# Optimization experiments

Measured on AMD Instinct MI355X. Metric: run time of the kernel, lower is better.

Reference implementation:

```python
import jax, jax.numpy as jnp
import numpy as np

B, S, D, H = 4, 1024, 1024, 16
DH = D // H  # head_dim = 64


def setup_inputs() -> dict:
    key = jax.random.key(0)
    kq, kk, kv, kl, kwq, kwk, kwv, kwo = jax.random.split(key, 8)
    query = jax.random.normal(kq, (B, S, D), dtype=jnp.float32)
    key_t = jax.random.normal(kk, (B, S, D), dtype=jnp.float32)
    value = jax.random.normal(kv, (B, S, D), dtype=jnp.float32)
    # padding: keys at positions >= valid length are padded (True)
    lengths = jax.random.randint(kl, (B,), S // 2, S + 1)
    key_padding_mask = jnp.arange(S)[None, :] >= lengths[:, None]  # [B,S] bool
    scale = 1.0 / np.sqrt(D)
    Wq = jax.random.normal(kwq, (D, D), dtype=jnp.float32) * scale
    Wk = jax.random.normal(kwk, (D, D), dtype=jnp.float32) * scale
    Wv = jax.random.normal(kwv, (D, D), dtype=jnp.float32) * scale
    Wo = jax.random.normal(kwo, (D, D), dtype=jnp.float32) * scale
    gamma = jnp.ones((H,), dtype=jnp.float32)
    return {"query": query, "key": key_t, "value": value,
            "key_padding_mask": key_padding_mask,
            "Wq": Wq, "Wk": Wk, "Wv": Wv, "Wo": Wo, "gamma": gamma}


def reference(query, key, value, key_padding_mask, Wq, Wk, Wv, Wo, gamma):
    # nn.Linear(x) = x @ W.T (bias=False)
    q = jnp.einsum('bsd,ed->bse', query, Wq).reshape(B, S, H, DH).transpose(0, 2, 1, 3)  # [B,H,S,Dh]
    k = jnp.einsum('bsd,ed->bse', key, Wk).reshape(B, S, H, DH).transpose(0, 2, 1, 3)
    v = jnp.einsum('bsd,ed->bse', value, Wv).reshape(B, S, H, DH).transpose(0, 2, 1, 3)
    scores = jnp.einsum('bhqd,bhkd->bhqk', q, k) / jnp.sqrt(jnp.float32(DH))
    pad = key_padding_mask[:, None, None, :]  # [B,1,1,S]
    scores = jnp.where(pad, -jnp.inf, scores)
    v = jnp.where(key_padding_mask[:, None, :, None], 0.0, v)
    attn = jax.nn.softmax(scores, axis=-1)  # dropout p=0 (eval) -> identity
    ws = jnp.einsum('bhqk,bhkd->bhqd', attn, v)
    ws = ws * gamma[None, :, None, None]  # per-head scale
    ws = ws.transpose(0, 2, 1, 3).reshape(B, S, D)
    return jnp.einsum('bsd,ed->bse', ws, Wo)
```

## Files before the change

### kernel.cpp

```cpp
#include <hip/hip_runtime.h>
#include <math.h>

#define S_LEN 1024
#define DMODEL 1024

typedef __attribute__((ext_vector_type(8))) short bf16x8;
typedef __attribute__((ext_vector_type(4))) short bf16x4;
typedef __attribute__((ext_vector_type(4))) float f32x4;

#define MFMA16(a, b, c) __builtin_amdgcn_mfma_f32_16x16x32_bf16(a, b, c, 0, 0, 0)

#define WP (1024u * 1024u)
#define XP (4u * 1024u * 1024u)

__device__ __forceinline__ unsigned short rne_bf16(float f) {
    unsigned u = __float_as_uint(f);
    u += 0x7FFFu + ((u >> 16) & 1u);
    return (unsigned short)(u >> 16);
}

__device__ __forceinline__ void split_rne(float f, unsigned short& h, unsigned short& l) {
    unsigned short hh = rne_bf16(f);
    float lf = f - __uint_as_float(((unsigned)hh) << 16);
    h = hh;
    l = rne_bf16(lf);
}

typedef const __attribute__((address_space(1))) unsigned int* gas_t;
typedef __attribute__((address_space(3))) unsigned int* las_t;
__device__ __forceinline__ void glds16(const void* g, void* l) {
    __builtin_amdgcn_global_load_lds((gas_t)g, (las_t)l, 16, 0, 0);
}

__global__ __launch_bounds__(256)
void convert_wx(const float* __restrict__ W0, const float* __restrict__ W1,
                const float* __restrict__ W2, const float* __restrict__ W3,
                const float* __restrict__ Xq, const float* __restrict__ Xk,
                const float* __restrict__ Xv,
                unsigned short* __restrict__ Wpl, unsigned short* __restrict__ Xbase) {
    int blk = blockIdx.x;
    if (blk < 4096) {
        const int which = blk >> 10;
        const float* W = which == 0 ? W0 : which == 1 ? W1 : which == 2 ? W2 : W3;
        int i = ((blk & 1023) * 256 + threadIdx.x) * 4;
        float4 f = *(const float4*)&W[i];
        if (which == 3) {
            unsigned short* hi = Wpl + 3 * WP;
            unsigned short* lo = Wpl + 4 * WP;
            bf16x4 h, l;
            unsigned short hh, ll;
            split_rne(f.x, hh, ll); h[0] = (short)hh; l[0] = (short)ll;
            split_rne(f.y, hh, ll); h[1] = (short)hh; l[1] = (short)ll;
            split_rne(f.z, hh, ll); h[2] = (short)hh; l[2] = (short)ll;
            split_rne(f.w, hh, ll); h[3] = (short)hh; l[3] = (short)ll;
            *(bf16x4*)&hi[i] = h;
            *(bf16x4*)&lo[i] = l;
        } else {
            unsigned short* hi = Wpl + (size_t)which * WP;
            bf16x4 h;
            h[0] = (short)rne_bf16(f.x);
            h[1] = (short)rne_bf16(f.y);
            h[2] = (short)rne_bf16(f.z);
            h[3] = (short)rne_bf16(f.w);
            *(bf16x4*)&hi[i] = h;
        }
    } else {
        blk -= 4096;
        const int which = blk >> 12;
        const float* X = which == 0 ? Xq : which == 1 ? Xk : Xv;
        unsigned short* Xr = Xbase + (size_t)which * XP;
        int i = ((blk & 4095) * 256 + threadIdx.x) * 4;
        float4 f = *(const float4*)&X[i];
        bf16x4 h;
        h[0] = (short)rne_bf16(f.x);
        h[1] = (short)rne_bf16(f.y);
        h[2] = (short)rne_bf16(f.z);
        h[3] = (short)rne_bf16(f.w);
        *(bf16x4*)&Xr[i] = h;
    }
}

__global__ __launch_bounds__(256)
void gemm_proj(const unsigned short* __restrict__ Xbase,
               const unsigned short* __restrict__ Wpl,
               unsigned short* __restrict__ Obase) {
    __shared__ unsigned short AS[128 * 32];
    __shared__ unsigned short BS[128 * 32];

    const int z = blockIdx.z;
    const unsigned short* A = Xbase + (size_t)z * XP;
    const unsigned short* B = Wpl + (size_t)z * WP;

    const int t = threadIdx.x, lane = t & 63, w = t >> 6;
    const int quad = lane >> 4, l15 = lane & 15;
    const int wr = w & 1, wc = w >> 1;
    const int rowBase = blockIdx.y * 128, colBase = blockIdx.x * 128;

    const unsigned short* gA[2];
    const unsigned short* gB[2];
    unsigned short* lA[2];
    unsigned short* lB[2];
    #pragma unroll
    for (int e = 0; e < 2; e++) {
        int row = w * 32 + e * 16 + (lane >> 2);
        int cg = (lane & 3) ^ ((row >> 1) & 3);
        gA[e] = A + (size_t)(rowBase + row) * 1024 + cg * 8;
        gB[e] = B + (size_t)(colBase + row) * 1024 + cg * 8;
        lA[e] = &AS[(w * 32 + e * 16) * 32];
        lB[e] = &BS[(w * 32 + e * 16) * 32];
    }

    int aAd[4], bAd[4];
    #pragma unroll
    for (int i = 0; i < 4; i++) {
        int ra = wr * 64 + i * 16 + l15;
        aAd[i] = ra * 32 + (quad ^ ((ra >> 1) & 3)) * 8;
        int rb = wc * 64 + i * 16 + l15;
        bAd[i] = rb * 32 + (quad ^ ((rb >> 1) & 3)) * 8;
    }

    f32x4 acc[4][4] = {};

    for (int kt = 0; kt < 32; kt++) {
        if (kt) __syncthreads();
        const int ko = kt * 32;
        glds16(gA[0] + ko, lA[0]);
        glds16(gA[1] + ko, lA[1]);
        glds16(gB[0] + ko, lB[0]);
        glds16(gB[1] + ko, lB[1]);
        __syncthreads();

        bf16x8 af[4], bfr[4];
        #pragma unroll
        for (int i = 0; i < 4; i++) af[i] = *(const bf16x8*)&AS[aAd[i]];
        #pragma unroll
        for (int j = 0; j < 4; j++) bfr[j] = *(const bf16x8*)&BS[bAd[j]];
        #pragma unroll
        for (int j = 0; j < 4; j++)
            #pragma unroll
            for (int i = 0; i < 4; i++)
                acc[i][j] = MFMA16(af[i], bfr[j], acc[i][j]);
    }

    unsigned short* O = Obase + (size_t)z * XP;
    #pragma unroll
    for (int i = 0; i < 4; i++)
        #pragma unroll
        for (int j = 0; j < 4; j++)
            #pragma unroll
            for (int r = 0; r < 4; r++) {
                int m = rowBase + wr * 64 + i * 16 + quad * 4 + r;
                int n = colBase + wc * 64 + j * 16 + l15;
                int bb = m >> 10, s = m & 1023, hh = n >> 6, dh = n & 63;
                size_t hb = ((size_t)(bb * 16 + hh)) << 16;
                unsigned short v = rne_bf16(acc[i][j][r]);
                if (z == 2) O[hb + (size_t)dh * 1024 + s] = v;
                else        O[hb + s * 64 + dh] = v;
            }
}

__global__ __launch_bounds__(256)
void gemm_out2(const unsigned short* __restrict__ A,
               const unsigned short* __restrict__ Bh, const unsigned short* __restrict__ Bl,
               float* __restrict__ Cf) {
    __shared__ unsigned short AS[128 * 32];
    __shared__ unsigned short BhS[64 * 32], BlS[64 * 32];

    const int t = threadIdx.x, lane = t & 63, w = t >> 6;
    const int quad = lane >> 4, l15 = lane & 15;
    const int wr = w & 1, wc = w >> 1;
    const int rowBase = blockIdx.y * 128, colBase = blockIdx.x * 64;

    const unsigned short* gA[2];
    unsigned short* lA[2];
    #pragma unroll
    for (int e = 0; e < 2; e++) {
        int row = w * 32 + e * 16 + (lane >> 2);
        int cg = (lane & 3) ^ ((row >> 1) & 3);
        gA[e] = A + (size_t)(rowBase + row) * 1024 + cg * 8;
        lA[e] = &AS[(w * 32 + e * 16) * 32];
    }
    const unsigned short *gBh, *gBl;
    unsigned short *lBh, *lBl;
    {
        int row = w * 16 + (lane >> 2);
        int cg = (lane & 3) ^ ((row >> 1) & 3);
        gBh = Bh + (size_t)(colBase + row) * 1024 + cg * 8;
        gBl = Bl + (size_t)(colBase + row) * 1024 + cg * 8;
        lBh = &BhS[(w * 16) * 32];
        lBl = &BlS[(w * 16) * 32];
    }

    int aAd[4], bAd[2];
    #pragma unroll
    for (int i = 0; i < 4; i++) {
        int ra = wr * 64 + i * 16 + l15;
        aAd[i] = ra * 32 + (quad ^ ((ra >> 1) & 3)) * 8;
    }
    #pragma unroll
    for (int j = 0; j < 2; j++) {
        int rb = wc * 32 + j * 16 + l15;
        bAd[j] = rb * 32 + (quad ^ ((rb >> 1) & 3)) * 8;
    }

    f32x4 acc[4][2] = {};

    for (int kt = 0; kt < 32; kt++) {
        if (kt) __syncthreads();
        const int ko = kt * 32;
        glds16(gA[0] + ko, lA[0]);
        glds16(gA[1] + ko, lA[1]);
        glds16(gBh + ko, lBh);
        glds16(gBl + ko, lBl);
        __syncthreads();

        bf16x8 af[4], bhf[2], blf[2];
        #pragma unroll
        for (int i = 0; i < 4; i++) af[i] = *(const bf16x8*)&AS[aAd[i]];
        #pragma unroll
        for (int j = 0; j < 2; j++) {
            bhf[j] = *(const bf16x8*)&BhS[bAd[j]];
            blf[j] = *(const bf16x8*)&BlS[bAd[j]];
        }
        #pragma unroll
        for (int j = 0; j < 2; j++)
            #pragma unroll
            for (int i = 0; i < 4; i++) {
                acc[i][j] = MFMA16(af[i], bhf[j], acc[i][j]);
                acc[i][j] = MFMA16(af[i], blf[j], acc[i][j]);
            }
    }

    #pragma unroll
    for (int i = 0; i < 4; i++)
        #pragma unroll
        for (int j = 0; j < 2; j++)
            #pragma unroll
            for (int r = 0; r < 4; r++) {
                int m = rowBase + wr * 64 + i * 16 + quad * 4 + r;
                int n = colBase + wc * 32 + j * 16 + l15;
                Cf[(size_t)m * 1024 + n] = acc[i][j][r];
            }
}

__global__ __launch_bounds__(256)
void attn_mfma(const unsigned short* __restrict__ Qr, const unsigned short* __restrict__ Kr,
               const unsigned short* __restrict__ Vt,
               const int* __restrict__ mask, const float* __restrict__ gamma,
               unsigned short* __restrict__ WSr) {
    __shared__ int maskS[1024];
    __shared__ unsigned short Ks[64 * 72];
    __shared__ unsigned short Vs[64 * 72];
    __shared__ unsigned short Ph[4 * 16 * 72];

    const int t = threadIdx.x, lane = t & 63, w = t >> 6;
    const int quad = lane >> 4, l15 = lane & 15;
    const int q0 = blockIdx.x * 64, h = blockIdx.y, b = blockIdx.z;
    const size_t hb = ((size_t)(b * 16 + h)) << 16;

    ((int4*)maskS)[t] = ((const int4*)(mask + b * 1024))[t];

    bf16x8 qhi[2];
    {
        const int qrow = q0 + w * 16 + l15;
        const size_t qb = hb + (size_t)qrow * 64 + quad * 8;
        qhi[0] = *(const bf16x8*)&Qr[qb];
        qhi[1] = *(const bf16x8*)&Qr[qb + 32];
    }

    f32x4 o[4] = {};
    float lsum[4] = {0.f, 0.f, 0.f, 0.f};

    __syncthreads();

    for (int jt = 0; jt < 16; jt++) {
        const int j0 = jt * 64;
        if (maskS[j0]) break;
        const bool partial = maskS[j0 + 63] != 0;
        __syncthreads();
        #pragma unroll
        for (int e = 0; e < 2; e++) {
            int lin = e * 256 + t;
            int c = lin & 7, row = lin >> 3;
            *(bf16x8*)&Ks[row * 72 + c * 8] =
                *(const bf16x8*)&Kr[hb + (size_t)(j0 + row) * 64 + c * 8];
            *(bf16x8*)&Vs[row * 72 + c * 8] =
                *(const bf16x8*)&Vt[hb + (size_t)row * 1024 + j0 + c * 8];
        }
        __syncthreads();

        f32x4 s4[4] = {};
        #pragma unroll
        for (int nj = 0; nj < 4; nj++) {
            int kr = (nj * 16 + l15) * 72 + quad * 8;
            #pragma unroll
            for (int kk = 0; kk < 2; kk++) {
                bf16x8 kv = *(const bf16x8*)&Ks[kr + kk * 32];
                s4[nj] = MFMA16(qhi[kk], kv, s4[nj]);
            }
        }

        if (partial) {
            #pragma unroll
            for (int nj = 0; nj < 4; nj++) {
                int mk = maskS[j0 + nj * 16 + l15];
                #pragma unroll
                for (int r = 0; r < 4; r++) {
                    float p = mk ? 0.f : __expf(s4[nj][r] * 0.125f);
                    lsum[r] += p;
                    Ph[(w * 16 + quad * 4 + r) * 72 + nj * 16 + l15] = rne_bf16(p);
                }
            }
        } else {
            #pragma unroll
            for (int nj = 0; nj < 4; nj++) {
                #pragma unroll
                for (int r = 0; r < 4; r++) {
                    float p = __expf(s4[nj][r] * 0.125f);
                    lsum[r] += p;
                    Ph[(w * 16 + quad * 4 + r) * 72 + nj * 16 + l15] = rne_bf16(p);
                }
            }
        }

        bf16x8 ph[2];
        #pragma unroll
        for (int ks = 0; ks < 2; ks++)
            ph[ks] = *(const bf16x8*)&Ph[(w * 16 + l15) * 72 + ks * 32 + quad * 8];
        #pragma unroll
        for (int dt = 0; dt < 4; dt++) {
            int vr = (dt * 16 + l15) * 72 + quad * 8;
            #pragma unroll
            for (int ks = 0; ks < 2; ks++) {
                bf16x8 vv = *(const bf16x8*)&Vs[vr + ks * 32];
                o[dt] = MFMA16(ph[ks], vv, o[dt]);
            }
        }
    }

    #pragma unroll
    for (int r = 0; r < 4; r++) {
        lsum[r] += __shfl_xor(lsum[r], 1);
        lsum[r] += __shfl_xor(lsum[r], 2);
        lsum[r] += __shfl_xor(lsum[r], 4);
        lsum[r] += __shfl_xor(lsum[r], 8);
    }

    const float g = gamma[h];
    #pragma unroll
    for (int r = 0; r < 4; r++) {
        const int qrow = q0 + w * 16 + quad * 4 + r;
        const float sc = g / lsum[r];
        const size_t base = ((size_t)b * 1024 + qrow) * 1024 + h * 64;
        #pragma unroll
        for (int dt = 0; dt < 4; dt++)
            WSr[base + dt * 16 + l15] = rne_bf16(o[dt][r] * sc);
    }
}

extern "C" void kernel_launch(void* const* d_in, const int* in_sizes, int n_in,
                              void* d_out, int out_size, void* d_ws, size_t ws_size,
                              hipStream_t stream) {
    const float* query = (const float*)d_in[0];
    const float* key   = (const float*)d_in[1];
    const float* value = (const float*)d_in[2];
    const int*   mask  = (const int*)d_in[3];
    const float* Wq    = (const float*)d_in[4];
    const float* Wk    = (const float*)d_in[5];
    const float* Wv    = (const float*)d_in[6];
    const float* Wo    = (const float*)d_in[7];
    const float* gamma = (const float*)d_in[8];
    float* out = (float*)d_out;

    unsigned short* u = (unsigned short*)d_ws;
    unsigned short* Xbase = u;
    unsigned short* Obase = u + 3 * XP;
    unsigned short* Wpl   = u + 6 * XP;
    unsigned short* WSr   = Xbase;
    unsigned short* Qr = Obase, *Kr = Obase + XP, *Vt = Obase + 2 * XP;
    unsigned short* Woh = Wpl + 3 * WP, *Wol = Wpl + 4 * WP;

    convert_wx<<<16384, 256, 0, stream>>>(Wq, Wk, Wv, Wo, query, key, value, Wpl, Xbase);

    gemm_proj<<<dim3(8, 32, 3), 256, 0, stream>>>(Xbase, Wpl, Obase);

    attn_mfma<<<dim3(16, 16, 4), 256, 0, stream>>>(Qr, Kr, Vt, mask, gamma, WSr);

    gemm_out2<<<dim3(16, 32), 256, 0, stream>>>(WSr, Woh, Wol, out);
}
```

Measured before the change: 211.9 us.

## Drop split-bf16 Wo, widen GEMM K-tile, pre-swizzle K/V for LDS-free attention

The output projection now uses a single bf16 copy of Wo instead of a hi/lo split pair, and reuses the same 128x128 GEMM kernel with a 64-wide K tile and a rotated LDS swizzle. The projection epilogue writes K and V in MFMA-fragment-ready layouts, so the attention kernel loads them straight from global memory into registers with no shared-memory staging or barriers. Attention also handles 32 query rows per wave (128 per block) to reuse K/V fragments. The cost is lower precision in the output projection and more register pressure in attention.

```diff
diff --git a/kernel.cpp b/kernel.cpp
--- a/kernel.cpp
+++ b/kernel.cpp
@@ -1,8 +1,5 @@
 #include <hip/hip_runtime.h>
 #include <math.h>
-
-#define S_LEN 1024
-#define DMODEL 1024
 
 typedef __attribute__((ext_vector_type(8))) short bf16x8;
 typedef __attribute__((ext_vector_type(4))) short bf16x4;
@@ -10,8 +7,8 @@
 
 #define MFMA16(a, b, c) __builtin_amdgcn_mfma_f32_16x16x32_bf16(a, b, c, 0, 0, 0)
 
-#define WP (1024u * 1024u)
-#define XP (4u * 1024u * 1024u)
+#define WPL (1024u * 1024u)
+#define XPL (4u * 1024u * 1024u)
 
 __device__ __forceinline__ unsigned short rne_bf16(float f) {
     unsigned u = __float_as_uint(f);
@@ -19,13 +16,6 @@
     return (unsigned short)(u >> 16);
 }
 
-__device__ __forceinline__ void split_rne(float f, unsigned short& h, unsigned short& l) {
-    unsigned short hh = rne_bf16(f);
-    float lf = f - __uint_as_float(((unsigned)hh) << 16);
-    h = hh;
-    l = rne_bf16(lf);
-}
-
 typedef const __attribute__((address_space(1))) unsigned int* gas_t;
 typedef __attribute__((address_space(3))) unsigned int* las_t;
 __device__ __forceinline__ void glds16(const void* g, void* l) {
@@ -33,243 +23,171 @@
 }
 
 __global__ __launch_bounds__(256)
-void convert_wx(const float* __restrict__ W0, const float* __restrict__ W1,
-                const float* __restrict__ W2, const float* __restrict__ W3,
-                const float* __restrict__ Xq, const float* __restrict__ Xk,
-                const float* __restrict__ Xv,
-                unsigned short* __restrict__ Wpl, unsigned short* __restrict__ Xbase) {
+void convert_all(const float* __restrict__ Wq, const float* __restrict__ Wk,
+                 const float* __restrict__ Wv, const float* __restrict__ Wo,
+                 const float* __restrict__ Xq, const float* __restrict__ Xk,
+                 const float* __restrict__ Xv,
+                 unsigned short* __restrict__ Wb, unsigned short* __restrict__ Xb) {
     int blk = blockIdx.x;
+    const float* S;
+    unsigned short* D;
     if (blk < 4096) {
-        const int which = blk >> 10;
-        const float* W = which == 0 ? W0 : which == 1 ? W1 : which == 2 ? W2 : W3;
-        int i = ((blk & 1023) * 256 + threadIdx.x) * 4;
-        float4 f = *(const float4*)&W[i];
-        if (which == 3) {
-            unsigned short* hi = Wpl + 3 * WP;
-            unsigned short* lo = Wpl + 4 * WP;
-            bf16x4 h, l;
-            unsigned short hh, ll;
-            split_rne(f.x, hh, ll); h[0] = (short)hh; l[0] = (short)ll;
-            split_rne(f.y, hh, ll); h[1] = (short)hh; l[1] = (short)ll;
-            split_rne(f.z, hh, ll); h[2] = (short)hh; l[2] = (short)ll;
-            split_rne(f.w, hh, ll); h[3] = (short)hh; l[3] = (short)ll;
-            *(bf16x4*)&hi[i] = h;
-            *(bf16x4*)&lo[i] = l;
-        } else {
-            unsigned short* hi = Wpl + (size_t)which * WP;
-            bf16x4 h;
-            h[0] = (short)rne_bf16(f.x);
-            h[1] = (short)rne_bf16(f.y);
-            h[2] = (short)rne_bf16(f.z);
-            h[3] = (short)rne_bf16(f.w);
-            *(bf16x4*)&hi[i] = h;
-        }
+        int which = blk >> 10;
+        S = which == 0 ? Wq : which == 1 ? Wk : which == 2 ? Wv : Wo;
+        D = Wb + (size_t)which * WPL;
+        blk &= 1023;
     } else {
         blk -= 4096;
-        const int which = blk >> 12;
-        const float* X = which == 0 ? Xq : which == 1 ? Xk : Xv;
-        unsigned short* Xr = Xbase + (size_t)which * XP;
-        int i = ((blk & 4095) * 256 + threadIdx.x) * 4;
-        float4 f = *(const float4*)&X[i];
-        bf16x4 h;
-        h[0] = (short)rne_bf16(f.x);
-        h[1] = (short)rne_bf16(f.y);
-        h[2] = (short)rne_bf16(f.z);
-        h[3] = (short)rne_bf16(f.w);
-        *(bf16x4*)&Xr[i] = h;
-    }
+        int which = blk >> 12;
+        S = which == 0 ? Xq : which == 1 ? Xk : Xv;
+        D = Xb + (size_t)which * XPL;
+        blk &= 4095;
+    }
+    int i = (blk * 256 + threadIdx.x) * 4;
+    float4 f = *(const float4*)&S[i];
+    bf16x4 h;
+    h[0] = (short)rne_bf16(f.x);
+    h[1] = (short)rne_bf16(f.y);
+    h[2] = (short)rne_bf16(f.z);
+    h[3] = (short)rne_bf16(f.w);
+    *(bf16x4*)&D[i] = h;
 }
 
 __global__ __launch_bounds__(256)
-void gemm_proj(const unsigned short* __restrict__ Xbase,
-               const unsigned short* __restrict__ Wpl,
-               unsigned short* __restrict__ Obase) {
-    __shared__ unsigned short AS[128 * 32];
-    __shared__ unsigned short BS[128 * 32];
-
-    const int z = blockIdx.z;
-    const unsigned short* A = Xbase + (size_t)z * XP;
-    const unsigned short* B = Wpl + (size_t)z * WP;
+void gemm_ab(const unsigned short* __restrict__ Abase,
+             const unsigned short* __restrict__ Bbase,
+             unsigned short* __restrict__ QKV, float* __restrict__ Cf,
+             int modeBase) {
+    __shared__ unsigned short AS[128 * 64], BS[128 * 64];
+    const int z = blockIdx.z, mode = modeBase + z;
+    const unsigned short* A = Abase + (size_t)z * XPL;
+    const unsigned short* B = Bbase + (size_t)z * WPL;
 
     const int t = threadIdx.x, lane = t & 63, w = t >> 6;
     const int quad = lane >> 4, l15 = lane & 15;
     const int wr = w & 1, wc = w >> 1;
     const int rowBase = blockIdx.y * 128, colBase = blockIdx.x * 128;
 
-    const unsigned short* gA[2];
-    const unsigned short* gB[2];
-    unsigned short* lA[2];
-    unsigned short* lB[2];
-    #pragma unroll
-    for (int e = 0; e < 2; e++) {
-        int row = w * 32 + e * 16 + (lane >> 2);
-        int cg = (lane & 3) ^ ((row >> 1) & 3);
+    const int srow = lane >> 3;
+    const int cg = ((lane & 7) + 2 * srow) & 7;
+    const unsigned short *gA[4], *gB[4];
+    unsigned short *lA[4], *lB[4];
+    #pragma unroll
+    for (int e = 0; e < 4; e++) {
+        int row = e * 32 + w * 8 + srow;
         gA[e] = A + (size_t)(rowBase + row) * 1024 + cg * 8;
         gB[e] = B + (size_t)(colBase + row) * 1024 + cg * 8;
-        lA[e] = &AS[(w * 32 + e * 16) * 32];
-        lB[e] = &BS[(w * 32 + e * 16) * 32];
-    }
-
-    int aAd[4], bAd[4];
+        lA[e] = &AS[(e * 32 + w * 8) * 64];
+        lB[e] = &BS[(e * 32 + w * 8) * 64];
+    }
+
+    const int s0 = (quad - 2 * l15) & 7;
+    const int c0 = s0 * 8, c1 = ((s0 + 4) & 7) * 8;
+    int aOff[4], bOff[4];
     #pragma unroll
     for (int i = 0; i < 4; i++) {
-        int ra = wr * 64 + i * 16 + l15;
-        aAd[i] = ra * 32 + (quad ^ ((ra >> 1) & 3)) * 8;
-        int rb = wc * 64 + i * 16 + l15;
-        bAd[i] = rb * 32 + (quad ^ ((rb >> 1) & 3)) * 8;
+        aOff[i] = (wr * 64 + i * 16 + l15) * 64;
+        bOff[i] = (wc * 64 + i * 16 + l15) * 64;
     }
 
     f32x4 acc[4][4] = {};
 
-    for (int kt = 0; kt < 32; kt++) {
+    for (int kt = 0; kt < 16; kt++) {
         if (kt) __syncthreads();
-        const int ko = kt * 32;
-        glds16(gA[0] + ko, lA[0]);
-        glds16(gA[1] + ko, lA[1]);
-        glds16(gB[0] + ko, lB[0]);
-        glds16(gB[1] + ko, lB[1]);
+        const int ko = kt * 64;
+        #pragma unroll
+        for (int e = 0; e < 4; e++) {
+            glds16(gA[e] + ko, lA[e]);
+            glds16(gB[e] + ko, lB[e]);
+        }
         __syncthreads();
 
         bf16x8 af[4], bfr[4];
         #pragma unroll
-        for (int i = 0; i < 4; i++) af[i] = *(const bf16x8*)&AS[aAd[i]];
-        #pragma unroll
-        for (int j = 0; j < 4; j++) bfr[j] = *(const bf16x8*)&BS[bAd[j]];
+        for (int i = 0; i < 4; i++) af[i] = *(const bf16x8*)&AS[aOff[i] + c0];
+        #pragma unroll
+        for (int j = 0; j < 4; j++) bfr[j] = *(const bf16x8*)&BS[bOff[j] + c0];
         #pragma unroll
         for (int j = 0; j < 4; j++)
             #pragma unroll
             for (int i = 0; i < 4; i++)
                 acc[i][j] = MFMA16(af[i], bfr[j], acc[i][j]);
-    }
-
-    unsigned short* O = Obase + (size_t)z * XP;
-    #pragma unroll
-    for (int i = 0; i < 4; i++)
+
+        #pragma unroll
+        for (int i = 0; i < 4; i++) af[i] = *(const bf16x8*)&AS[aOff[i] + c1];
+        #pragma unroll
+        for (int j = 0; j < 4; j++) bfr[j] = *(const bf16x8*)&BS[bOff[j] + c1];
         #pragma unroll
         for (int j = 0; j < 4; j++)
             #pragma unroll
-            for (int r = 0; r < 4; r++) {
-                int m = rowBase + wr * 64 + i * 16 + quad * 4 + r;
-                int n = colBase + wc * 64 + j * 16 + l15;
-                int bb = m >> 10, s = m & 1023, hh = n >> 6, dh = n & 63;
-                size_t hb = ((size_t)(bb * 16 + hh)) << 16;
-                unsigned short v = rne_bf16(acc[i][j][r]);
-                if (z == 2) O[hb + (size_t)dh * 1024 + s] = v;
-                else        O[hb + s * 64 + dh] = v;
-            }
+            for (int i = 0; i < 4; i++)
+                acc[i][j] = MFMA16(af[i], bfr[j], acc[i][j]);
+    }
+
+    if (mode == 3) {
+        #pragma unroll
+        for (int i = 0; i < 4; i++)
+            #pragma unroll
+            for (int j = 0; j < 4; j++)
+                #pragma unroll
+                for (int r = 0; r < 4; r++) {
+                    int m = rowBase + wr * 64 + i * 16 + quad * 4 + r;
+                    int n = colBase + wc * 64 + j * 16 + l15;
+                    Cf[(size_t)m * 1024 + n] = acc[i][j][r];
+                }
+    } else {
+        unsigned short* O = QKV + (size_t)z * XPL;
+        #pragma unroll
+        for (int i = 0; i < 4; i++)
+            #pragma unroll
+            for (int j = 0; j < 4; j++)
+                #pragma unroll
+                for (int r = 0; r < 4; r++) {
+                    int m = rowBase + wr * 64 + i * 16 + quad * 4 + r;
+                    int n = colBase + wc * 64 + j * 16 + l15;
+                    int bb = m >> 10, s = m & 1023, hh = n >> 6, dh = n & 63;
+                    size_t hb = ((size_t)(bb * 16 + hh)) << 16;
+                    unsigned short v = rne_bf16(acc[i][j][r]);
+                    if (mode == 0) {
+                        O[hb + s * 64 + dh] = v;
+                    } else if (mode == 1) {
+                        O[hb + (size_t)((s >> 4) * 2 + (dh >> 5)) * 512 +
+                          ((dh >> 3) & 3) * 128 + (s & 15) * 8 + (dh & 7)] = v;
+                    } else {
+                        O[hb + (size_t)((dh >> 4) * 32 + (s >> 5)) * 512 +
+                          ((s >> 3) & 3) * 128 + (dh & 15) * 8 + (s & 7)] = v;
+                    }
+                }
+    }
 }
 
 __global__ __launch_bounds__(256)
-void gemm_out2(const unsigned short* __restrict__ A,
-               const unsigned short* __restrict__ Bh, const unsigned short* __restrict__ Bl,
-               float* __restrict__ Cf) {
-    __shared__ unsigned short AS[128 * 32];
-    __shared__ unsigned short BhS[64 * 32], BlS[64 * 32];
-
-    const int t = threadIdx.x, lane = t & 63, w = t >> 6;
-    const int quad = lane >> 4, l15 = lane & 15;
-    const int wr = w & 1, wc = w >> 1;
-    const int rowBase = blockIdx.y * 128, colBase = blockIdx.x * 64;
-
-    const unsigned short* gA[2];
-    unsigned short* lA[2];
-    #pragma unroll
-    for (int e = 0; e < 2; e++) {
-        int row = w * 32 + e * 16 + (lane >> 2);
-        int cg = (lane & 3) ^ ((row >> 1) & 3);
-        gA[e] = A + (size_t)(rowBase + row) * 1024 + cg * 8;
-        lA[e] = &AS[(w * 32 + e * 16) * 32];
-    }
-    const unsigned short *gBh, *gBl;
-    unsigned short *lBh, *lBl;
-    {
-        int row = w * 16 + (lane >> 2);
-        int cg = (lane & 3) ^ ((row >> 1) & 3);
-        gBh = Bh + (size_t)(colBase + row) * 1024 + cg * 8;
-        gBl = Bl + (size_t)(colBase + row) * 1024 + cg * 8;
-        lBh = &BhS[(w * 16) * 32];
-        lBl = &BlS[(w * 16) * 32];
-    }
-
-    int aAd[4], bAd[2];
-    #pragma unroll
-    for (int i = 0; i < 4; i++) {
-        int ra = wr * 64 + i * 16 + l15;
-        aAd[i] = ra * 32 + (quad ^ ((ra >> 1) & 3)) * 8;
-    }
-    #pragma unroll
-    for (int j = 0; j < 2; j++) {
-        int rb = wc * 32 + j * 16 + l15;
-        bAd[j] = rb * 32 + (quad ^ ((rb >> 1) & 3)) * 8;
-    }
-
-    f32x4 acc[4][2] = {};
-
-    for (int kt = 0; kt < 32; kt++) {
-        if (kt) __syncthreads();
-        const int ko = kt * 32;
-        glds16(gA[0] + ko, lA[0]);
-        glds16(gA[1] + ko, lA[1]);
-        glds16(gBh + ko, lBh);
-        glds16(gBl + ko, lBl);
-        __syncthreads();
-
-        bf16x8 af[4], bhf[2], blf[2];
-        #pragma unroll
-        for (int i = 0; i < 4; i++) af[i] = *(const bf16x8*)&AS[aAd[i]];
-        #pragma unroll
-        for (int j = 0; j < 2; j++) {
-            bhf[j] = *(const bf16x8*)&BhS[bAd[j]];
-            blf[j] = *(const bf16x8*)&BlS[bAd[j]];
-        }
-        #pragma unroll
-        for (int j = 0; j < 2; j++)
-            #pragma unroll
-            for (int i = 0; i < 4; i++) {
-                acc[i][j] = MFMA16(af[i], bhf[j], acc[i][j]);
-                acc[i][j] = MFMA16(af[i], blf[j], acc[i][j]);
-            }
-    }
-
-    #pragma unroll
-    for (int i = 0; i < 4; i++)
-        #pragma unroll
-        for (int j = 0; j < 2; j++)
-            #pragma unroll
-            for (int r = 0; r < 4; r++) {
-                int m = rowBase + wr * 64 + i * 16 + quad * 4 + r;
-                int n = colBase + wc * 32 + j * 16 + l15;
-                Cf[(size_t)m * 1024 + n] = acc[i][j][r];
-            }
-}
-
-__global__ __launch_bounds__(256)
-void attn_mfma(const unsigned short* __restrict__ Qr, const unsigned short* __restrict__ Kr,
-               const unsigned short* __restrict__ Vt,
+void attn_flat(const unsigned short* __restrict__ Qp,
+               const unsigned short* __restrict__ Kf,
+               const unsigned short* __restrict__ Vf,
                const int* __restrict__ mask, const float* __restrict__ gamma,
                unsigned short* __restrict__ WSr) {
     __shared__ int maskS[1024];
-    __shared__ unsigned short Ks[64 * 72];
-    __shared__ unsigned short Vs[64 * 72];
-    __shared__ unsigned short Ph[4 * 16 * 72];
+    __shared__ unsigned short Ph[4][32 * 72];
 
     const int t = threadIdx.x, lane = t & 63, w = t >> 6;
     const int quad = lane >> 4, l15 = lane & 15;
-    const int q0 = blockIdx.x * 64, h = blockIdx.y, b = blockIdx.z;
+    const int q0 = blockIdx.x * 128, h = blockIdx.y, b = blockIdx.z;
     const size_t hb = ((size_t)(b * 16 + h)) << 16;
 
     ((int4*)maskS)[t] = ((const int4*)(mask + b * 1024))[t];
 
-    bf16x8 qhi[2];
-    {
-        const int qrow = q0 + w * 16 + l15;
-        const size_t qb = hb + (size_t)qrow * 64 + quad * 8;
-        qhi[0] = *(const bf16x8*)&Qr[qb];
-        qhi[1] = *(const bf16x8*)&Qr[qb + 32];
-    }
-
-    f32x4 o[4] = {};
-    float lsum[4] = {0.f, 0.f, 0.f, 0.f};
+    bf16x8 qf[2][2];
+    #pragma unroll
+    for (int mi = 0; mi < 2; mi++) {
+        size_t qb = hb + (size_t)(q0 + w * 32 + mi * 16 + l15) * 64 + quad * 8;
+        qf[mi][0] = *(const bf16x8*)&Qp[qb];
+        qf[mi][1] = *(const bf16x8*)&Qp[qb + 32];
+    }
+
+    f32x4 o[2][4] = {};
+    float lsum[2][4] = {{0.f, 0.f, 0.f, 0.f}, {0.f, 0.f, 0.f, 0.f}};
+    unsigned short* P = Ph[w];
 
     __syncthreads();
 
@@ -277,85 +195,84 @@
         const int j0 = jt * 64;
         if (maskS[j0]) break;
         const bool partial = maskS[j0 + 63] != 0;
-        __syncthreads();
-        #pragma unroll
-        for (int e = 0; e < 2; e++) {
-            int lin = e * 256 + t;
-            int c = lin & 7, row = lin >> 3;
-            *(bf16x8*)&Ks[row * 72 + c * 8] =
-                *(const bf16x8*)&Kr[hb + (size_t)(j0 + row) * 64 + c * 8];
-            *(bf16x8*)&Vs[row * 72 + c * 8] =
-                *(const bf16x8*)&Vt[hb + (size_t)row * 1024 + j0 + c * 8];
-        }
-        __syncthreads();
-
-        f32x4 s4[4] = {};
-        #pragma unroll
-        for (int nj = 0; nj < 4; nj++) {
-            int kr = (nj * 16 + l15) * 72 + quad * 8;
-            #pragma unroll
-            for (int kk = 0; kk < 2; kk++) {
-                bf16x8 kv = *(const bf16x8*)&Ks[kr + kk * 32];
-                s4[nj] = MFMA16(qhi[kk], kv, s4[nj]);
-            }
-        }
-
-        if (partial) {
+
+        bf16x8 kv[4][2];
+        #pragma unroll
+        for (int nj = 0; nj < 4; nj++)
+            #pragma unroll
+            for (int kk = 0; kk < 2; kk++)
+                kv[nj][kk] = *(const bf16x8*)&Kf[hb + (size_t)((jt * 4 + nj) * 2 + kk) * 512 + lane * 8];
+
+        f32x4 s4[2][4] = {};
+        #pragma unroll
+        for (int nj = 0; nj < 4; nj++)
+            #pragma unroll
+            for (int kk = 0; kk < 2; kk++)
+                #pragma unroll
+                for (int mi = 0; mi < 2; mi++)
+                    s4[mi][nj] = MFMA16(qf[mi][kk], kv[nj][kk], s4[mi][nj]);
+
+        bf16x8 vv[4][2];
+        #pragma unroll
+        for (int dt = 0; dt < 4; dt++)
+            #pragma unroll
+            for (int ks = 0; ks < 2; ks++)
+                vv[dt][ks] = *(const bf16x8*)&Vf[hb + (size_t)(dt * 32 + jt * 2 + ks) * 512 + lane * 8];
+
+        #pragma unroll
+        for (int mi = 0; mi < 2; mi++)
             #pragma unroll
             for (int nj = 0; nj < 4; nj++) {
-                int mk = maskS[j0 + nj * 16 + l15];
+                int mk = partial ? maskS[j0 + nj * 16 + l15] : 0;
                 #pragma unroll
                 for (int r = 0; r < 4; r++) {
-                    float p = mk ? 0.f : __expf(s4[nj][r] * 0.125f);
-                    lsum[r] += p;
-                    Ph[(w * 16 + quad * 4 + r) * 72 + nj * 16 + l15] = rne_bf16(p);
+                    float p = mk ? 0.f : __expf(s4[mi][nj][r] * 0.125f);
+                    lsum[mi][r] += p;
+                    int rowW = mi * 16 + quad * 4 + r;
+                    int slot = ((nj * 2 + (l15 >> 3)) - 2 * rowW) & 7;
+                    P[rowW * 72 + slot * 8 + (l15 & 7)] = rne_bf16(p);
                 }
             }
-        } else {
-            #pragma unroll
-            for (int nj = 0; nj < 4; nj++) {
-                #pragma unroll
-                for (int r = 0; r < 4; r++) {
-                    float p = __expf(s4[nj][r] * 0.125f);
-                    lsum[r] += p;
-                    Ph[(w * 16 + quad * 4 + r) * 72 + nj * 16 + l15] = rne_bf16(p);
-                }
-            }
+
+        bf16x8 pf[2][2];
+        #pragma unroll
+        for (int mi = 0; mi < 2; mi++) {
+            int rowR = mi * 16 + l15;
+            int sl0 = (quad - 2 * rowR) & 7;
+            pf[mi][0] = *(const bf16x8*)&P[rowR * 72 + sl0 * 8];
+            pf[mi][1] = *(const bf16x8*)&P[rowR * 72 + ((sl0 + 4) & 7) * 8];
         }
-
-        bf16x8 ph[2];
-        #pragma unroll
-        for (int ks = 0; ks < 2; ks++)
-            ph[ks] = *(const bf16x8*)&Ph[(w * 16 + l15) * 72 + ks * 32 + quad * 8];
-        #pragma unroll
-        for (int dt = 0; dt < 4; dt++) {
-            int vr = (dt * 16 + l15) * 72 + quad * 8;
-            #pragma unroll
-            for (int ks = 0; ks < 2; ks++) {
-                bf16x8 vv = *(const bf16x8*)&Vs[vr + ks * 32];
-                o[dt] = MFMA16(ph[ks], vv, o[dt]);
-            }
+        #pragma unroll
+        for (int dt = 0; dt < 4; dt++)
+            #pragma unroll
+            for (int ks = 0; ks < 2; ks++)
+                #pragma unroll
+                for (int mi = 0; mi < 2; mi++)
+                    o[mi][dt] = MFMA16(pf[mi][ks], vv[dt][ks], o[mi][dt]);
+    }
+
+    #pragma unroll
+    for (int mi = 0; mi < 2; mi++)
+        #pragma unroll
+        for (int r = 0; r < 4; r++) {
+            lsum[mi][r] += __shfl_xor(lsum[mi][r], 1);
+            lsum[mi][r] += __shfl_xor(lsum[mi][r], 2);
+            lsum[mi][r] += __shfl_xor(lsum[mi][r], 4);
+            lsum[mi][r] += __shfl_xor(lsum[mi][r], 8);
         }
-    }
-
-    #pragma unroll
-    for (int r = 0; r < 4; r++) {
-        lsum[r] += __shfl_xor(lsum[r], 1);
-        lsum[r] += __shfl_xor(lsum[r], 2);
-        lsum[r] += __shfl_xor(lsum[r], 4);
-        lsum[r] += __shfl_xor(lsum[r], 8);
-    }
 
     const float g = gamma[h];
     #pragma unroll
-    for (int r = 0; r < 4; r++) {
-        const int qrow = q0 + w * 16 + quad * 4 + r;
-        const float sc = g / lsum[r];
-        const size_t base = ((size_t)b * 1024 + qrow) * 1024 + h * 64;
-        #pragma unroll
-        for (int dt = 0; dt < 4; dt++)
-            WSr[base + dt * 16 + l15] = rne_bf16(o[dt][r] * sc);
-    }
+    for (int mi = 0; mi < 2; mi++)
+        #pragma unroll
+        for (int r = 0; r < 4; r++) {
+            int qrow = q0 + w * 32 + mi * 16 + quad * 4 + r;
+            float sc = g / lsum[mi][r];
+            size_t base = ((size_t)b * 1024 + qrow) * 1024 + h * 64;
+            #pragma unroll
+            for (int dt = 0; dt < 4; dt++)
+                WSr[base + dt * 16 + l15] = rne_bf16(o[mi][dt][r] * sc);
+        }
 }
 
 extern "C" void kernel_launch(void* const* d_in, const int* in_sizes, int n_in,
@@ -373,18 +290,18 @@
     float* out = (float*)d_out;
 
     unsigned short* u = (unsigned short*)d_ws;
-    unsigned short* Xbase = u;
-    unsigned short* Obase = u + 3 * XP;
-    unsigned short* Wpl   = u + 6 * XP;
-    unsigned short* WSr   = Xbase;
-    unsigned short* Qr = Obase, *Kr = Obase + XP, *Vt = Obase + 2 * XP;
-    unsigned short* Woh = Wpl + 3 * WP, *Wol = Wpl + 4 * WP;
-
-    convert_wx<<<16384, 256, 0, stream>>>(Wq, Wk, Wv, Wo, query, key, value, Wpl, Xbase);
-
-    gemm_proj<<<dim3(8, 32, 3), 256, 0, stream>>>(Xbase, Wpl, Obase);
-
-    attn_mfma<<<dim3(16, 16, 4), 256, 0, stream>>>(Qr, Kr, Vt, mask, gamma, WSr);
-
-    gemm_out2<<<dim3(16, 32), 256, 0, stream>>>(WSr, Woh, Wol, out);
-}
+    unsigned short* Xb  = u;
+    unsigned short* QKV = u + 3 * XPL;
+    unsigned short* Wb  = u + 6 * XPL;
+    unsigned short* WSr = Xb;
+    unsigned short* Qp = QKV, *Kfp = QKV + XPL, *Vfp = QKV + 2 * XPL;
+    unsigned short* Wob = Wb + 3 * WPL;
+
+    convert_all<<<16384, 256, 0, stream>>>(Wq, Wk, Wv, Wo, query, key, value, Wb, Xb);
+
+    gemm_ab<<<dim3(8, 32, 3), 256, 0, stream>>>(Xb, Wb, QKV, nullptr, 0);
+
+    attn_flat<<<dim3(8, 16, 4), 256, 0, stream>>>(Qp, Kfp, Vfp, mask, gamma, WSr);
+
+    gemm_ab<<<dim3(8, 32, 1), 256, 0, stream>>>(WSr, Wob, nullptr, out, 3);
+}
```

Result: slower. 217.1 us (+2.4%).
